# Kernel tuning notes

Measured on AMD Instinct MI355X. Metric: run time of the kernel, lower is better.

## Reference

```python
import jax, jax.numpy as jnp
import numpy as np

N = 512   # particles
T = 128   # timesteps
V_L = 3.4
V_0 = 4.2
GAMMA = 0.9
ALPHA = 0.15
BETA = 15.0
E_CRIT_INV = 2e-5
F_STD = 0.05
G_STD = 0.02
NU = 1.0 / (G_STD * float(np.sqrt(2.0 * np.pi)))
CUR_MIN = 0.0
CUR_MAX = 1.0


def voc(soc):
    # open-circuit voltage model
    return (V_L + (V_0 - V_L) * jnp.exp(GAMMA * (soc - 1.0))
            + ALPHA * V_L * (soc - 1.0)
            + (1.0 - ALPHA) * V_L * (jnp.exp(-BETA) - jnp.exp(-BETA * jnp.sqrt(soc))))


def mlp(x, w1, b1, w2, b2, w3, b3):
    h = jax.nn.sigmoid(x @ w1 + b1)
    h = jax.nn.sigmoid(h @ w2 + b2)
    return h @ w3 + b3


def setup_inputs() -> dict:
    key = jax.random.key(0)
    ks = jax.random.split(key, 11)
    soc_init = jax.random.uniform(ks[0], (N, 1), jnp.float32, 0.6, 1.0)
    current = jax.random.uniform(ks[1], (1, T), jnp.float32)
    voltage_measured = 3.4 + 0.8 * jax.random.uniform(ks[2], (1, T), jnp.float32)
    noise = jax.random.normal(ks[3], (T, N, 1), jnp.float32)
    u = jax.random.uniform(ks[4], (T,), jnp.float32)
    w1 = jax.random.normal(ks[5], (2, 1024), jnp.float32) / np.float32(np.sqrt(2.0))
    b1 = jnp.zeros((1024,), jnp.float32)
    w2 = jax.random.normal(ks[6], (1024, 512), jnp.float32) / np.float32(np.sqrt(1024.0))
    b2 = jnp.zeros((512,), jnp.float32)
    w3 = jax.random.normal(ks[7], (512, 1), jnp.float32) / np.float32(np.sqrt(512.0))
    b3 = jnp.zeros((1,), jnp.float32)
    return {"soc_init": soc_init, "current": current, "voltage_measured": voltage_measured,
            "noise": noise, "u": u, "w1": w1, "b1": b1, "w2": w2, "b2": b2, "w3": w3, "b3": b3}


def reference(soc_init, current, voltage_measured, noise, u, w1, b1, w2, b2, w3, b3):
    n = soc_init.shape[0]
    # pre-loop step: V at t=0 conditions
    I0 = current[0, 0] * jnp.ones_like(soc_init)
    sI0 = (I0 - CUR_MIN) / (CUR_MAX - CUR_MIN)
    Z0 = mlp(jnp.concatenate([soc_init, sI0], axis=1), w1, b1, w2, b2, w3, b3)
    V0 = voc(soc_init) - I0 * Z0

    log_n = jnp.log(jnp.float32(n))

    def step(carry, xs):
        soc, I, V = carry
        cur_t, vmeas_t, noise_t, u_t = xs
        # state propagation with process noise, then clamp to (0, 1]
        soc = soc - I * V * E_CRIT_INV + F_STD * noise_t
        soc = jnp.where(soc > 1.0, 1.0, jnp.where(soc < 0.0, 1e-10, soc))
        I = cur_t * jnp.ones_like(soc)
        sI = (I - CUR_MIN) / (CUR_MAX - CUR_MIN)
        Z = mlp(jnp.concatenate([soc, sI], axis=1), w1, b1, w2, b2, w3, b3)  # [N,1]
        V = voc(soc) - I * Z                                                 # [N,1]
        # importance weights / step loss (logsumexp trick as in source)
        logW = jnp.log(jnp.float32(NU)) - 0.5 * jnp.square((V - vmeas_t) / G_STD)
        step_loss = jax.nn.logsumexp(logW) - log_n
        # systematic resampling on normalized weights
        wn = jax.nn.softmax(logW[:, 0])          # normalized weights [N]
        cum = jnp.cumsum(wn)
        pos = (jnp.arange(n, dtype=jnp.float32) + u_t) / jnp.float32(n)
        idx = jnp.clip(jnp.searchsorted(cum, pos), 0, n - 1)
        soc_r = soc[idx]
        return (soc_r, I, V), (V[:, 0], soc_r[:, 0], step_loss)

    xs = (current[0], voltage_measured[0], noise, u)
    _, (v_hist, s_hist, losses) = jax.lax.scan(step, (soc_init, I0, V0), xs)
    loss = jnp.sum(losses)
    voltage = v_hist.T    # [N, T]
    soc_hist = s_hist.T   # [N, T]
    return loss, voltage, soc_hist
```

## Files before the change

kernel.cpp:

```cpp
#include <hip/hip_runtime.h>
#include <math.h>

#define NP 512
#define TS 128
#define GI 33
#define TAB2D (GI * GI)
#define GV 193
#define V_Lc 3.4f
#define V_0c 4.2f
#define GAMMAc 0.9f
#define ALPHAc 0.15f
#define BETAc 15.0f
#define E_INV 2e-5f
#define F_STDc 0.05f
#define G_STDc 0.02f

#define LBAR() asm volatile("s_waitcnt lgkmcnt(0)\n\ts_barrier" ::: "memory")

__device__ __forceinline__ float sigmoid_jax(float x) {
    float e = expf(-fabsf(x));
    float num = (x >= 0.f) ? 1.f : e;
    return num / (1.f + e);
}

__device__ __forceinline__ float vocf(float s) {
    float sm1 = s - 1.f;
    return V_Lc + (V_0c - V_Lc) * expf(GAMMAc * sm1)
         + (ALPHAc * V_Lc) * sm1
         + (1.f - ALPHAc) * V_Lc * (expf(-BETAc) - expf(-BETAc * sqrtf(s)));
}

template <int R>
__device__ __forceinline__ int dpp_ror(int v) {
    return __builtin_amdgcn_update_dpp(0, v, 0x120 | R, 0xf, 0xf, false);
}
template <int S>
__device__ __forceinline__ int dpp_shr(int v) {
    return __builtin_amdgcn_update_dpp(0, v, 0x110 | S, 0xf, 0xf, true);
}
__device__ __forceinline__ float rdlane_f(float v, int l) {
    return __int_as_float(__builtin_amdgcn_readlane(__float_as_int(v), l));
}

__device__ __forceinline__ float wave_max_f(float v) {
    v = fmaxf(v, __int_as_float(dpp_ror<1>(__float_as_int(v))));
    v = fmaxf(v, __int_as_float(dpp_ror<2>(__float_as_int(v))));
    v = fmaxf(v, __int_as_float(dpp_ror<4>(__float_as_int(v))));
    v = fmaxf(v, __int_as_float(dpp_ror<8>(__float_as_int(v))));
    int iv = __float_as_int(v);
    v = fmaxf(v, __int_as_float(__builtin_amdgcn_update_dpp(iv, iv, 0x142, 0xf, 0xf, false)));
    iv = __float_as_int(v);
    v = fmaxf(v, __int_as_float(__builtin_amdgcn_update_dpp(iv, iv, 0x143, 0xf, 0xf, false)));
    return rdlane_f(v, 63);
}

__device__ __forceinline__ int wave_max_i(int v) {
    v = max(v, dpp_ror<1>(v));
    v = max(v, dpp_ror<2>(v));
    v = max(v, dpp_ror<4>(v));
    v = max(v, dpp_ror<8>(v));
    v = max(v, __builtin_amdgcn_update_dpp(v, v, 0x142, 0xf, 0xf, false));
    v = max(v, __builtin_amdgcn_update_dpp(v, v, 0x143, 0xf, 0xf, false));
    return __builtin_amdgcn_readlane(v, 63);
}

__device__ __forceinline__ float wave_scan_add(float v, int lane) {
    v += __int_as_float(dpp_shr<1>(__float_as_int(v)));
    v += __int_as_float(dpp_shr<2>(__float_as_int(v)));
    v += __int_as_float(dpp_shr<4>(__float_as_int(v)));
    v += __int_as_float(dpp_shr<8>(__float_as_int(v)));
    float s15 = rdlane_f(v, 15);
    float s31 = rdlane_f(v, 31);
    float s47 = rdlane_f(v, 47);
    int row = lane >> 4;
    if (row >= 1) v += s15;
    if (row >= 2) v += s31;
    if (row >= 3) v += s47;
    return v;
}

__device__ __forceinline__ int wave_scanmax_i(int v, int lane) {
    v = max(v, dpp_shr<1>(v));
    v = max(v, dpp_shr<2>(v));
    v = max(v, dpp_shr<4>(v));
    v = max(v, dpp_shr<8>(v));
    int r15 = __builtin_amdgcn_readlane(v, 15);
    int r31 = __builtin_amdgcn_readlane(v, 31);
    int r47 = __builtin_amdgcn_readlane(v, 47);
    int row = lane >> 4;
    if (row >= 1) v = max(v, r15);
    if (row >= 2) v = max(v, r31);
    if (row >= 3) v = max(v, r47);
    return v;
}

__device__ __forceinline__ float interp33(const float* __restrict__ row, float s) {
    float x = s * 32.0f;
    int j = (int)floorf(x);
    j = j < 0 ? 0 : (j > 31 ? 31 : j);
    int st = j - 1;
    st = st < 0 ? 0 : (st > 29 ? 29 : st);
    float uu = x - (float)st;
    float um0 = uu, um1 = uu - 1.f, um2 = uu - 2.f, um3 = uu - 3.f;
    float c0 = um1 * um2 * um3 * (-1.f / 6.f);
    float c1 = um0 * um2 * um3 * (0.5f);
    float c2 = um0 * um1 * um3 * (-0.5f);
    float c3 = um0 * um1 * um2 * (1.f / 6.f);
    return c0 * row[st] + c1 * row[st + 1] + c2 * row[st + 2] + c3 * row[st + 3];
}

__device__ __forceinline__ float interp193(const float* __restrict__ row, float s) {
    float x = s * 192.0f;
    int j = (int)floorf(x);
    j = j < 0 ? 0 : (j > 191 ? 191 : j);
    int st = j - 1;
    st = st < 0 ? 0 : (st > 189 ? 189 : st);
    float uu = x - (float)st;
    float um0 = uu, um1 = uu - 1.f, um2 = uu - 2.f, um3 = uu - 3.f;
    float c0 = um1 * um2 * um3 * (-1.f / 6.f);
    float c1 = um0 * um2 * um3 * (0.5f);
    float c2 = um0 * um1 * um3 * (-0.5f);
    float c3 = um0 * um1 * um2 * (1.f / 6.f);
    return c0 * row[st] + c1 * row[st + 1] + c2 * row[st + 2] + c3 * row[st + 3];
}

__device__ __forceinline__ int count_le(float C, float u) {
    int h = (int)floorf(C - u);
    h = h < -1 ? -1 : (h > 511 ? 511 : h);
    h += (int)((h < 511) && (((float)(h + 1) + u) <= C));
    h -= (int)((h >= 0) && (((float)h + u) > C));
    return h + 1;
}

#define BKT 32
__global__ __launch_bounds__(256) void k_tab(
    const float* __restrict__ w1, const float* __restrict__ b1,
    const float* __restrict__ w2, const float* __restrict__ b2,
    const float* __restrict__ w3, float* __restrict__ zpart)
{
    const int tid = threadIdx.x;
    const int rowblk = blockIdx.x >> 1;
    const int colhalf = blockIdx.x & 1;
    const int r0 = rowblk * 8;
    const int cbase = colhalf * 256;

    __shared__ float As[8][BKT + 1];
    __shared__ float Bs[BKT][256];
    __shared__ float srow[8], irow[8];

    if (tid < 8) {
        int r = r0 + tid;
        r = r > (TAB2D - 1) ? (TAB2D - 1) : r;
        int si = r / GI;
        int ii = r - si * GI;
        srow[tid] = (float)si * (1.0f / 32.0f);
        irow[tid] = (float)ii * (1.0f / 32.0f);
    }
    __syncthreads();

    const int rg = tid >> 5;
    const int ct = tid & 31;
    float acc[8];
    #pragma unroll
    for (int b = 0; b < 8; ++b) acc[b] = 0.f;

    for (int kk = 0; kk < 1024; kk += BKT) {
        {
            int kc = kk + ct;
            float pre = srow[rg] * w1[kc] + irow[rg] * w1[1024 + kc] + b1[kc];
            As[rg][ct] = sigmoid_jax(pre);
        }
        #pragma unroll
        for (int jj = 0; jj < 8; ++jj) {
            int vi = tid + jj * 256;
            int k = vi >> 6, c4 = vi & 63;
            *(float4*)&Bs[k][c4 * 4] = *(const float4*)&w2[(kk + k) * 512 + cbase + c4 * 4];
        }
        __syncthreads();
        #pragma unroll
        for (int k = 0; k < BKT; ++k) {
            float a = As[rg][k];
            float bq[8];
            *(float4*)&bq[0] = *(const float4*)&Bs[k][ct * 4];
            *(float4*)&bq[4] = *(const float4*)&Bs[k][ct * 4 + 128];
            #pragma unroll
            for (int q = 0; q < 8; ++q) acc[q] += a * bq[q];
        }
        __syncthreads();
    }

    float b2r[8], w3r[8];
    *(float4*)&b2r[0] = *(const float4*)&b2[cbase + ct * 4];
    *(float4*)&b2r[4] = *(const float4*)&b2[cbase + ct * 4 + 128];
    *(float4*)&w3r[0] = *(const float4*)&w3[cbase + ct * 4];
    *(float4*)&w3r[4] = *(const float4*)&w3[cbase + ct * 4 + 128];
    float zp = 0.f;
    #pragma unroll
    for (int q = 0; q < 8; ++q)
        zp += w3r[q] * sigmoid_jax(acc[q] + b2r[q]);
    #pragma unroll
    for (int mm = 1; mm < 32; mm <<= 1) zp += __shfl_xor(zp, mm);
    if (ct == 0 && (r0 + rg) < TAB2D)
        zpart[colhalf * TAB2D + r0 + rg] = zp;
}

__global__ __launch_bounds__(512, 1) void k_seq(
    const float* __restrict__ zpart, const float* __restrict__ soc_init,
    const float* __restrict__ current, const float* __restrict__ vmeas,
    const float* __restrict__ u, const float* __restrict__ noise,
    const float* __restrict__ b3, float* __restrict__ vbuf,
    float* __restrict__ sbuf, float* __restrict__ out)
{
    const int tid = threadIdx.x;
    const int lane = tid & 63;
    const int wv = tid >> 6;

    __shared__ float vt[TS][GV];
    __shared__ float zt[TS][GI];
    __shared__ float zt2d[TAB2D];
    __shared__ float vocs[GV];
    __shared__ float socs[2][NP];
    __shared__ int marker[NP];
    __shared__ float cur_s[TS], vm_s[TS], u_s[TS];
    __shared__ float redM[8], redT[8];

    float bb3 = b3[0];
    for (int j = tid; j < TAB2D; j += 512) zt2d[j] = zpart[j] + zpart[TAB2D + j] + bb3;
    if (tid < TS) { cur_s[tid] = current[tid]; vm_s[tid] = vmeas[tid]; u_s[tid] = u[tid]; }
    if (tid < GV) vocs[tid] = vocf((float)tid * (1.0f / 192.0f));
    marker[tid] = 0;
    __syncthreads();
    for (int idx = tid; idx < TS * GI; idx += 512) {
        int t = idx / GI, g = idx - t * GI;
        zt[t][g] = interp33(&zt2d[g * GI], cur_s[t]);
    }
    __syncthreads();
    for (int idx = tid; idx < TS * GV; idx += 512) {
        int t = idx / GV, j = idx - t * GV;
        float sj = (float)j * (1.0f / 192.0f);
        vt[t][j] = vocs[j] - cur_s[t] * interp33(&zt[t][0], sj);
    }
    __syncthreads();

    float soc = soc_init[tid];
    float Iprev = cur_s[0];
    float V = interp193(&vt[0][0], soc);
    float loss_acc = 0.f;
    const float LOG_NU = logf(19.947114020071635f);
    const float LOG_N = logf(512.f);
    float nz_cur = noise[tid];

    for (int t = 0; t < TS; ++t) {
        int tn = (t + 1 < TS) ? t + 1 : t;
        float nz_next = noise[tn * 512 + tid];

        soc = soc - Iprev * V * E_INV + F_STDc * nz_cur;
        soc = soc > 1.f ? 1.f : (soc < 0.f ? 1e-10f : soc);
        socs[t & 1][tid] = soc;

        V = interp193(&vt[t][0], soc);
        float d = (V - vm_s[t]) * (1.f / G_STDc);
        float lw = LOG_NU - 0.5f * d * d;

        float m = wave_max_f(lw);
        float e = __expf(lw - m);
        float incl = wave_scan_add(e, lane);
        if (lane == 63) { redM[wv] = m; redT[wv] = incl; }
        LBAR();

        float rm = redM[lane & 7];
        float rt = redT[lane & 7];
        float M = rm;
        M = fmaxf(M, __int_as_float(dpp_ror<1>(__float_as_int(M))));
        M = fmaxf(M, __int_as_float(dpp_ror<2>(__float_as_int(M))));
        M = fmaxf(M, __int_as_float(dpp_ror<4>(__float_as_int(M))));
        M = fmaxf(M, __int_as_float(dpp_ror<8>(__float_as_int(M))));
        float fw = __expf(rm - M);
        float term = rt * fw;
        float sc = term;
        sc += __int_as_float(dpp_shr<1>(__float_as_int(sc)));
        sc += __int_as_float(dpp_shr<2>(__float_as_int(sc)));
        sc += __int_as_float(dpp_shr<4>(__float_as_int(sc)));
        float S = rdlane_f(sc, 7);
        float off = 0.f;
        if (wv > 0) off = rdlane_f(sc, wv - 1);
        float fw_own = rdlane_f(fw, wv);
        loss_acc += M + __logf(S) - LOG_N;

        float C = 512.f * ((off + incl * fw_own) / S);
        int hi = count_le(C, u_s[t]);
        if (hi < 512) atomicMax(&marker[hi], (t << 10) | (tid + 1));
        LBAR();

        int pm = 0;
        for (int w = 0; w < wv; ++w) pm = max(pm, marker[w * 64 + lane]);
        pm = wave_max_i(pm);
        int v = wave_scanmax_i(marker[tid], lane);
        int sv = max(v, pm);
        int owner = ((sv >> 10) == t) ? (sv & 1023) : 0;
        owner = owner > 511 ? 511 : owner;
        float socr = socs[t & 1][owner];

        vbuf[t * 512 + tid] = V;
        sbuf[t * 512 + tid] = socr;
        soc = socr;
        Iprev = cur_s[t];
        nz_cur = nz_next;
    }
    if (tid == 0) out[0] = loss_acc;
}

__global__ __launch_bounds__(256) void k_fin(
    const float* __restrict__ vbuf, const float* __restrict__ sbuf,
    float* __restrict__ out)
{
    __shared__ float tile[32][33];
    int tz = blockIdx.z;
    int t0 = blockIdx.x * 32;
    int i0 = blockIdx.y * 32;
    const float* src = tz ? sbuf : vbuf;
    float* dst = out + 1 + tz * (NP * TS);
    int tx = threadIdx.x & 31, ty = threadIdx.x >> 5;
    #pragma unroll
    for (int m2 = 0; m2 < 4; ++m2)
        tile[ty + 8 * m2][tx] = src[(t0 + ty + 8 * m2) * 512 + i0 + tx];
    __syncthreads();
    #pragma unroll
    for (int m2 = 0; m2 < 4; ++m2)
        dst[(i0 + ty + 8 * m2) * 128 + t0 + tx] = tile[tx][ty + 8 * m2];
}

extern "C" void kernel_launch(void* const* d_in, const int* in_sizes, int n_in,
                              void* d_out, int out_size, void* d_ws, size_t ws_size,
                              hipStream_t stream)
{
    const float* soc_init = (const float*)d_in[0];
    const float* current  = (const float*)d_in[1];
    const float* vmeas    = (const float*)d_in[2];
    const float* noise    = (const float*)d_in[3];
    const float* u        = (const float*)d_in[4];
    const float* w1 = (const float*)d_in[5];
    const float* b1 = (const float*)d_in[6];
    const float* w2 = (const float*)d_in[7];
    const float* b2 = (const float*)d_in[8];
    const float* w3 = (const float*)d_in[9];
    const float* b3 = (const float*)d_in[10];
    float* out = (float*)d_out;
    float* ws  = (float*)d_ws;

    float* zpart = ws;
    float* vbuf  = ws + 2180;
    float* sbuf  = vbuf + NP * TS;

    k_tab<<<274, 256, 0, stream>>>(w1, b1, w2, b2, w3, zpart);
    k_seq<<<1, 512, 0, stream>>>(zpart, soc_init, current, vmeas, u, noise, b3,
                                 vbuf, sbuf, out);
    k_fin<<<dim3(4, 16, 2), 256, 0, stream>>>(vbuf, sbuf, out);
}
```

Measured before the change: 265.2 us.

## Write outputs transposed from sequential kernel and double rows per table block

Removes the separate transpose kernel: the sequential particle-filter kernel now writes voltage and SOC histories directly into the [N,T] output layout, so one launch and an extra global round-trip go away. The stores become strided (each thread writes along its own row), which may be less coalesced inside the serial loop. The table-building MLP kernel now computes 16 rows per block with two accumulators per thread, halving the grid and reusing each loaded w2 tile for twice as many rows.

Measured after the change: 285.1 us. 1.07x slower.

```diff
diff --git a/kernel.cpp b/kernel.cpp
--- a/kernel.cpp
+++ b/kernel.cpp
@@ -141,14 +141,14 @@
     const int tid = threadIdx.x;
     const int rowblk = blockIdx.x >> 1;
     const int colhalf = blockIdx.x & 1;
-    const int r0 = rowblk * 8;
+    const int r0 = rowblk * 16;
     const int cbase = colhalf * 256;
 
-    __shared__ float As[8][BKT + 1];
+    __shared__ float As[16][BKT + 1];
     __shared__ float Bs[BKT][256];
-    __shared__ float srow[8], irow[8];
-
-    if (tid < 8) {
+    __shared__ float srow[16], irow[16];
+
+    if (tid < 16) {
         int r = r0 + tid;
         r = r > (TAB2D - 1) ? (TAB2D - 1) : r;
         int si = r / GI;
@@ -160,15 +160,19 @@
 
     const int rg = tid >> 5;
     const int ct = tid & 31;
-    float acc[8];
+    float acc[2][8];
     #pragma unroll
-    for (int b = 0; b < 8; ++b) acc[b] = 0.f;
+    for (int a = 0; a < 2; ++a)
+        #pragma unroll
+        for (int b = 0; b < 8; ++b) acc[a][b] = 0.f;
 
     for (int kk = 0; kk < 1024; kk += BKT) {
-        {
-            int kc = kk + ct;
-            float pre = srow[rg] * w1[kc] + irow[rg] * w1[1024 + kc] + b1[kc];
-            As[rg][ct] = sigmoid_jax(pre);
+        #pragma unroll
+        for (int h = 0; h < 2; ++h) {
+            int idx = tid + h * 256;
+            int row = idx >> 5, k = idx & 31, kc = kk + k;
+            float pre = srow[row] * w1[kc] + irow[row] * w1[1024 + kc] + b1[kc];
+            As[row][k] = sigmoid_jax(pre);
         }
         #pragma unroll
         for (int jj = 0; jj < 8; ++jj) {
@@ -179,12 +183,16 @@
         __syncthreads();
         #pragma unroll
         for (int k = 0; k < BKT; ++k) {
-            float a = As[rg][k];
+            float a0 = As[rg * 2][k];
+            float a1 = As[rg * 2 + 1][k];
             float bq[8];
             *(float4*)&bq[0] = *(const float4*)&Bs[k][ct * 4];
             *(float4*)&bq[4] = *(const float4*)&Bs[k][ct * 4 + 128];
             #pragma unroll
-            for (int q = 0; q < 8; ++q) acc[q] += a * bq[q];
+            for (int q = 0; q < 8; ++q) {
+                acc[0][q] += a0 * bq[q];
+                acc[1][q] += a1 * bq[q];
+            }
         }
         __syncthreads();
     }
@@ -194,22 +202,24 @@
     *(float4*)&b2r[4] = *(const float4*)&b2[cbase + ct * 4 + 128];
     *(float4*)&w3r[0] = *(const float4*)&w3[cbase + ct * 4];
     *(float4*)&w3r[4] = *(const float4*)&w3[cbase + ct * 4 + 128];
-    float zp = 0.f;
     #pragma unroll
-    for (int q = 0; q < 8; ++q)
-        zp += w3r[q] * sigmoid_jax(acc[q] + b2r[q]);
-    #pragma unroll
-    for (int mm = 1; mm < 32; mm <<= 1) zp += __shfl_xor(zp, mm);
-    if (ct == 0 && (r0 + rg) < TAB2D)
-        zpart[colhalf * TAB2D + r0 + rg] = zp;
+    for (int rr = 0; rr < 2; ++rr) {
+        float zp = 0.f;
+        #pragma unroll
+        for (int q = 0; q < 8; ++q)
+            zp += w3r[q] * sigmoid_jax(acc[rr][q] + b2r[q]);
+        #pragma unroll
+        for (int mm = 1; mm < 32; mm <<= 1) zp += __shfl_xor(zp, mm);
+        if (ct == 0 && (r0 + rg * 2 + rr) < TAB2D)
+            zpart[colhalf * TAB2D + r0 + rg * 2 + rr] = zp;
+    }
 }
 
 __global__ __launch_bounds__(512, 1) void k_seq(
     const float* __restrict__ zpart, const float* __restrict__ soc_init,
     const float* __restrict__ current, const float* __restrict__ vmeas,
     const float* __restrict__ u, const float* __restrict__ noise,
-    const float* __restrict__ b3, float* __restrict__ vbuf,
-    float* __restrict__ sbuf, float* __restrict__ out)
+    const float* __restrict__ b3, float* __restrict__ out)
 {
     const int tid = threadIdx.x;
     const int lane = tid & 63;
@@ -249,6 +259,8 @@
     const float LOG_NU = logf(19.947114020071635f);
     const float LOG_N = logf(512.f);
     float nz_cur = noise[tid];
+    float* outV = out + 1 + tid * TS;
+    float* outS = out + 1 + NP * TS + tid * TS;
 
     for (int t = 0; t < TS; ++t) {
         int tn = (t + 1 < TS) ? t + 1 : t;
@@ -301,33 +313,13 @@
         owner = owner > 511 ? 511 : owner;
         float socr = socs[t & 1][owner];
 
-        vbuf[t * 512 + tid] = V;
-        sbuf[t * 512 + tid] = socr;
+        outV[t] = V;
+        outS[t] = socr;
         soc = socr;
         Iprev = cur_s[t];
         nz_cur = nz_next;
     }
     if (tid == 0) out[0] = loss_acc;
-}
-
-__global__ __launch_bounds__(256) void k_fin(
-    const float* __restrict__ vbuf, const float* __restrict__ sbuf,
-    float* __restrict__ out)
-{
-    __shared__ float tile[32][33];
-    int tz = blockIdx.z;
-    int t0 = blockIdx.x * 32;
-    int i0 = blockIdx.y * 32;
-    const float* src = tz ? sbuf : vbuf;
-    float* dst = out + 1 + tz * (NP * TS);
-    int tx = threadIdx.x & 31, ty = threadIdx.x >> 5;
-    #pragma unroll
-    for (int m2 = 0; m2 < 4; ++m2)
-        tile[ty + 8 * m2][tx] = src[(t0 + ty + 8 * m2) * 512 + i0 + tx];
-    __syncthreads();
-    #pragma unroll
-    for (int m2 = 0; m2 < 4; ++m2)
-        dst[(i0 + ty + 8 * m2) * 128 + t0 + tx] = tile[tx][ty + 8 * m2];
 }
 
 extern "C" void kernel_launch(void* const* d_in, const int* in_sizes, int n_in,
@@ -349,11 +341,7 @@
     float* ws  = (float*)d_ws;
 
     float* zpart = ws;
-    float* vbuf  = ws + 2180;
-    float* sbuf  = vbuf + NP * TS;
-
-    k_tab<<<274, 256, 0, stream>>>(w1, b1, w2, b2, w3, zpart);
-    k_seq<<<1, 512, 0, stream>>>(zpart, soc_init, current, vmeas, u, noise, b3,
-                                 vbuf, sbuf, out);
-    k_fin<<<dim3(4, 16, 2), 256, 0, stream>>>(vbuf, sbuf, out);
-}
+
+    k_tab<<<138, 256, 0, stream>>>(w1, b1, w2, b2, w3, zpart);
+    k_seq<<<1, 512, 0, stream>>>(zpart, soc_init, current, vmeas, u, noise, b3, out);
+}
```
